# Optimization experiments

Measured on AMD Instinct MI355X. Metric: run time of the kernel, lower is better.

## Reference

```python
import jax, jax.numpy as jnp
import numpy as np

H = 12          # num heads
D = 768         # hidden size
DH = D // H     # size per head
FF = 3072       # intermediate size
EPS = 1e-11


def gelu(x):
    # tanh approximation, matching the TF source exactly
    c = np.sqrt(2.0 / np.pi).astype(np.float32)
    return x * 0.5 * (1.0 + jnp.tanh(c * (x + 0.044715 * jnp.power(x, 3))))


def layer_norm(x, gamma, beta):
    mean = jnp.mean(x, axis=-1, keepdims=True)
    var = jnp.mean(jnp.square(x - mean), axis=-1, keepdims=True)
    return (x - mean) * jax.lax.rsqrt(var + EPS) * gamma + beta


def setup_inputs() -> dict:
    key = jax.random.key(0)
    ks = jax.random.split(key, 12)
    B, S = 16, 512
    std = 0.02
    inp = {
        "x": jax.random.normal(ks[0], (B, S, D), jnp.float32),
        "mask": jnp.ones((B, S), dtype=bool),
        "Wq": jax.random.normal(ks[1], (D, D), jnp.float32) * std,
        "bq": jnp.zeros((D,), jnp.float32),
        "Wk": jax.random.normal(ks[2], (D, D), jnp.float32) * std,
        "bk": jnp.zeros((D,), jnp.float32),
        "Wv": jax.random.normal(ks[3], (D, D), jnp.float32) * std,
        "bv": jnp.zeros((D,), jnp.float32),
        "Wo": jax.random.normal(ks[4], (D, D), jnp.float32) * std,
        "bo": jnp.zeros((D,), jnp.float32),
        "g1": jnp.ones((D,), jnp.float32),
        "b1": jnp.zeros((D,), jnp.float32),
        "Wi": jax.random.normal(ks[5], (D, FF), jnp.float32) * std,
        "bi": jnp.zeros((FF,), jnp.float32),
        "Wo2": jax.random.normal(ks[6], (FF, D), jnp.float32) * std,
        "bo2": jnp.zeros((D,), jnp.float32),
        "g2": jnp.ones((D,), jnp.float32),
        "b2": jnp.zeros((D,), jnp.float32),
    }
    return inp


def reference(x, mask, Wq, bq, Wk, bk, Wv, bv, Wo, bo, g1, b1, Wi, bi, Wo2, bo2, g2, b2):
    B, S, _ = x.shape
    # QKV projections
    q = (x @ Wq + bq).reshape(B, S, H, DH)
    k = (x @ Wk + bk).reshape(B, S, H, DH)
    v = (x @ Wv + bv).reshape(B, S, H, DH)
    # scaled dot-product attention scores [B, H, S, S]
    scores = jnp.einsum("bqhd,bkhd->bhqk", q, k) / np.sqrt(DH).astype(np.float32)
    # key-side mask, applied as score * m + (1 - m) * -100 (per original source)
    m = mask[:, None, None, :].astype(jnp.float32)
    scores = scores * m + (1.0 - m) * (-100.0)
    probs = jax.nn.softmax(scores, axis=-1)
    attn = jnp.einsum("bhqk,bkhd->bqhd", probs, v).reshape(B, S, D)
    # tf.boolean_mask with all-True mask -> flatten batch and seq dims
    attn = attn.reshape(B * S, D)
    x_flat = x.reshape(B * S, D)
    # attention output projection + residual + LN
    attn_out = layer_norm(attn @ Wo + bo + x_flat, g1, b1)
    # FFN: gelu dense then output dense + residual + LN
    inter = gelu(attn_out @ Wi + bi)
    out = layer_norm(inter @ Wo2 + bo2 + attn_out, g2, b2)
    return out
```

## Files before the change

### kernel.cpp

```cpp
#include <hip/hip_runtime.h>


#define DEV __device__ __forceinline__

typedef unsigned short u16;
typedef unsigned int   u32;
typedef __bf16 bf16x8 __attribute__((ext_vector_type(8)));
typedef float  f32x4  __attribute__((ext_vector_type(4)));
typedef unsigned short u16x8 __attribute__((ext_vector_type(8)));
typedef unsigned short u16x4 __attribute__((ext_vector_type(4)));

DEV u16 f2bf(float f) {
    u32 u = __builtin_bit_cast(u32, f);
    u += 0x7fffu + ((u >> 16) & 1u);
    return (u16)(u >> 16);
}

DEV float gelu_f(float x) {
    float u = 0.7978845608028654f * (x + 0.044715f * x * x * x);
    float e = __expf(2.f * u);
    return 0.5f * x * (2.f - 2.f / (e + 1.f));
}

DEV void gload16(const void* gsrc, void* ldst) {
    __builtin_amdgcn_global_load_lds(
        (__attribute__((address_space(1))) void*)(void*)(const_cast<void*>(gsrc)),
        (__attribute__((address_space(3))) void*)ldst, 16, 0, 0);
}

DEV f32x4 MFMA(bf16x8 a, bf16x8 b, f32x4 c) {
    return __builtin_amdgcn_mfma_f32_16x16x32_bf16(a, b, c, 0, 0, 0);
}

__global__ __launch_bounds__(256) void cvt_bf16(const float* __restrict__ in,
                                                u16* __restrict__ out, int n) {
    int i = (blockIdx.x * 256 + threadIdx.x) * 4;
    if (i >= n) return;
    f32x4 v = *(const f32x4*)(in + i);
    u16x4 o;
    o.x = f2bf(v.x); o.y = f2bf(v.y); o.z = f2bf(v.z); o.w = f2bf(v.w);
    *(u16x4*)(out + i) = o;
}

__global__ __launch_bounds__(256) void transpose_cvt(const float* __restrict__ in,
                                                     u16* __restrict__ out,
                                                     int R, int C) {
    __shared__ float tile[32][33];
    int tx = threadIdx.x & 31, ty = threadIdx.x >> 5;
    int r0 = blockIdx.y * 32, c0 = blockIdx.x * 32;
#pragma unroll
    for (int i = 0; i < 4; i++)
        tile[ty + i * 8][tx] = in[(size_t)(r0 + ty + i * 8) * C + c0 + tx];
    __syncthreads();
#pragma unroll
    for (int i = 0; i < 4; i++)
        out[(size_t)(c0 + ty + i * 8) * R + r0 + tx] = f2bf(tile[tx][ty + i * 8]);
}

__global__ void concat_bias(const float* __restrict__ bq, const float* __restrict__ bk,
                            const float* __restrict__ bv, float* __restrict__ o) {
    int i = blockIdx.x * 256 + threadIdx.x;
    if (i < 2304) o[i] = (i < 768) ? bq[i] : (i < 1536 ? bk[i - 768] : bv[i - 1536]);
}

template <int EPI>
__global__ __launch_bounds__(256) void gemm_bt(const u16* __restrict__ A,
                                               const u16* __restrict__ BT,
                                               const float* __restrict__ bias,
                                               void* __restrict__ Cout,
                                               int N, int K) {
    __shared__ __align__(16) char smem[32768];
    const int t = threadIdx.x, lane = t & 63, wid = t >> 6;
    const int tm = blockIdx.y, tn = blockIdx.x;
    const int wm = wid >> 1, wn = wid & 1;

    f32x4 acc[4][4];
#pragma unroll
    for (int i = 0; i < 4; i++)
#pragma unroll
        for (int j = 0; j < 4; j++) acc[i][j] = f32x4{0.f, 0.f, 0.f, 0.f};

    const u16* Ab = A + (size_t)tm * 128 * K;
    const u16* Bb = BT + (size_t)tn * 128 * K;
    char* As = smem;
    char* Bs = smem + 16384;

    for (int kt = 0; kt < K; kt += 64) {
        __syncthreads();
#pragma unroll
        for (int i = 0; i < 4; i++) {
            int cw = wid * 4 + i;
            int o = cw * 1024 + lane * 16;
            int row = o >> 7;
            int cb = (o & 127) ^ ((row & 7) << 4);
            gload16(Ab + (size_t)row * K + kt + (cb >> 1), As + cw * 1024);
            gload16(Bb + (size_t)row * K + kt + (cb >> 1), Bs + cw * 1024);
        }
        __syncthreads();
#pragma unroll
        for (int ks = 0; ks < 2; ++ks) {
            bf16x8 af[4], bfr[4];
#pragma unroll
            for (int mi = 0; mi < 4; mi++) {
                int row = wm * 64 + mi * 16 + (lane & 15);
                int cb = (ks * 64 + ((lane >> 4) << 4)) ^ ((row & 7) << 4);
                af[mi] = *(const bf16x8*)(As + row * 128 + cb);
            }
#pragma unroll
            for (int ni = 0; ni < 4; ni++) {
                int row = wn * 64 + ni * 16 + (lane & 15);
                int cb = (ks * 64 + ((lane >> 4) << 4)) ^ ((row & 7) << 4);
                bfr[ni] = *(const bf16x8*)(Bs + row * 128 + cb);
            }
#pragma unroll
            for (int mi = 0; mi < 4; mi++)
#pragma unroll
                for (int ni = 0; ni < 4; ni++)
                    acc[mi][ni] = MFMA(af[mi], bfr[ni], acc[mi][ni]);
        }
    }

    const int r0 = tm * 128 + wm * 64, c0 = tn * 128 + wn * 64;
    float bcol[4];
#pragma unroll
    for (int ni = 0; ni < 4; ni++) bcol[ni] = bias[c0 + ni * 16 + (lane & 15)];
#pragma unroll
    for (int mi = 0; mi < 4; mi++) {
#pragma unroll
        for (int r = 0; r < 4; r++) {
            int gr = r0 + mi * 16 + ((lane >> 4) << 2) + r;
#pragma unroll
            for (int ni = 0; ni < 4; ni++) {
                int gc = c0 + ni * 16 + (lane & 15);
                float v = acc[mi][ni][r] + bcol[ni];
                if constexpr (EPI == 2) v = gelu_f(v);
                if constexpr (EPI == 1)
                    ((float*)Cout)[(size_t)gr * N + gc] = v;
                else
                    ((u16*)Cout)[(size_t)gr * N + gc] = f2bf(v);
            }
        }
    }
}

__global__ __launch_bounds__(256) void attn_kernel(const u16* __restrict__ QKV,
                                                   u16* __restrict__ attnb) {
    __shared__ __align__(16) char sm[24576];
    char* Ks = sm;
    char* Vt = sm + 8192;
    const int t = threadIdx.x, lane = t & 63, wid = t >> 6;
    const int qt = blockIdx.x, bh = blockIdx.y;
    const int b = bh / 12, h = bh % 12;
    const size_t base = (size_t)b * 512 * 2304;
    char* Pw = sm + 16384 + wid * 2048;

    bf16x8 aq[2];
    {
        int qrow = qt * 64 + wid * 16 + (lane & 15);
        const u16* qp = QKV + base + (size_t)qrow * 2304 + h * 64 + ((lane >> 4) << 3);
        aq[0] = *(const bf16x8*)qp;
        aq[1] = *(const bf16x8*)(qp + 32);
    }
    f32x4 oacc[4];
#pragma unroll
    for (int g = 0; g < 4; g++) oacc[g] = f32x4{0.f, 0.f, 0.f, 0.f};
    float mrun[4] = {-1e30f, -1e30f, -1e30f, -1e30f};
    float lrun[4] = {0.f, 0.f, 0.f, 0.f};

    for (int kt = 0; kt < 8; ++kt) {
        __syncthreads();
#pragma unroll
        for (int i = 0; i < 2; i++) {
            int cw = wid * 2 + i;
            int o = cw * 1024 + lane * 16;
            int row = o >> 7;
            int cb = (o & 127) ^ ((row & 7) << 4);
            gload16(QKV + base + (size_t)(kt * 64 + row) * 2304 + 768 + h * 64 + (cb >> 1),
                    Ks + cw * 1024);
        }
        {
            int key = t & 63, dh0 = wid * 16;
            const u16* vp = QKV + base + (size_t)(kt * 64 + key) * 2304 + 1536 + h * 64 + dh0;
            u16x8 v0 = *(const u16x8*)vp;
            u16x8 v1 = *(const u16x8*)(vp + 8);
#pragma unroll
            for (int j = 0; j < 8; j++) {
                int dh = dh0 + j;
                *(u16*)(Vt + dh * 128 + ((key * 2) ^ ((dh & 7) << 4))) = v0[j];
            }
#pragma unroll
            for (int j = 0; j < 8; j++) {
                int dh = dh0 + 8 + j;
                *(u16*)(Vt + dh * 128 + ((key * 2) ^ ((dh & 7) << 4))) = v1[j];
            }
        }
        __syncthreads();

        f32x4 sacc[4];
#pragma unroll
        for (int ni = 0; ni < 4; ni++) sacc[ni] = f32x4{0.f, 0.f, 0.f, 0.f};
#pragma unroll
        for (int ni = 0; ni < 4; ni++) {
            int row = ni * 16 + (lane & 15);
#pragma unroll
            for (int ks = 0; ks < 2; ks++) {
                int cb = (ks * 64 + ((lane >> 4) << 4)) ^ ((row & 7) << 4);
                bf16x8 bk = *(const bf16x8*)(Ks + row * 128 + cb);
                sacc[ni] = MFMA(aq[ks], bk, sacc[ni]);
            }
        }
#pragma unroll
        for (int ni = 0; ni < 4; ni++)
#pragma unroll
            for (int r = 0; r < 4; r++) sacc[ni][r] *= 0.125f;

#pragma unroll
        for (int r = 0; r < 4; r++) {
            float pm = fmaxf(fmaxf(sacc[0][r], sacc[1][r]), fmaxf(sacc[2][r], sacc[3][r]));
            pm = fmaxf(pm, __shfl_xor(pm, 1));
            pm = fmaxf(pm, __shfl_xor(pm, 2));
            pm = fmaxf(pm, __shfl_xor(pm, 4));
            pm = fmaxf(pm, __shfl_xor(pm, 8));
            float mnew = fmaxf(mrun[r], pm);
            float sf = __expf(mrun[r] - mnew);
            mrun[r] = mnew;
            lrun[r] *= sf;
#pragma unroll
            for (int g = 0; g < 4; g++) oacc[g][r] *= sf;
            int prow = ((lane >> 4) << 2) + r;
            float ps = 0.f;
#pragma unroll
            for (int ni = 0; ni < 4; ni++) {
                float p = __expf(sacc[ni][r] - mnew);
                ps += p;
                int col = ni * 16 + (lane & 15);
                *(u16*)(Pw + prow * 128 + ((col * 2) ^ ((prow & 7) << 4))) = f2bf(p);
            }
            ps += __shfl_xor(ps, 1);
            ps += __shfl_xor(ps, 2);
            ps += __shfl_xor(ps, 4);
            ps += __shfl_xor(ps, 8);
            lrun[r] += ps;
        }
        __syncthreads();

#pragma unroll
        for (int ks = 0; ks < 2; ks++) {
            int prow = lane & 15;
            int pcb = (ks * 64 + ((lane >> 4) << 4)) ^ ((prow & 7) << 4);
            bf16x8 ap = *(const bf16x8*)(Pw + prow * 128 + pcb);
#pragma unroll
            for (int g = 0; g < 4; g++) {
                int vrow = g * 16 + (lane & 15);
                int vcb = (ks * 64 + ((lane >> 4) << 4)) ^ ((vrow & 7) << 4);
                bf16x8 bv = *(const bf16x8*)(Vt + vrow * 128 + vcb);
                oacc[g] = MFMA(ap, bv, oacc[g]);
            }
        }
    }

#pragma unroll
    for (int g = 0; g < 4; g++)
#pragma unroll
        for (int r = 0; r < 4; r++) {
            int qrow = qt * 64 + wid * 16 + ((lane >> 4) << 2) + r;
            float o = oacc[g][r] / lrun[r];
            attnb[(size_t)(b * 512 + qrow) * 768 + h * 64 + g * 16 + (lane & 15)] = f2bf(o);
        }
}

__global__ __launch_bounds__(256) void ln_kernel(const float* __restrict__ Y,
                                                 const float* __restrict__ res,
                                                 const float* __restrict__ g,
                                                 const float* __restrict__ bta,
                                                 float* __restrict__ outf,
                                                 u16* __restrict__ outb) {
    int row = blockIdx.x, t = threadIdx.x, lane = t & 63, wid = t >> 6;
    const float* y = Y + (size_t)row * 768;
    const float* rr = res + (size_t)row * 768;
    float v[3];
#pragma unroll
    for (int i = 0; i < 3; i++) v[i] = y[t + i * 256] + rr[t + i * 256];

    float s = v[0] + v[1] + v[2];
#pragma unroll
    for (int o = 32; o; o >>= 1) s += __shfl_xor(s, o);
    __shared__ float sm[4];
    __shared__ float bc[2];
    if (lane == 0) sm[wid] = s;
    __syncthreads();
    if (t == 0) bc[0] = (sm[0] + sm[1] + sm[2] + sm[3]) * (1.f / 768.f);
    __syncthreads();
    float mean = bc[0];

    float q = 0.f;
#pragma unroll
    for (int i = 0; i < 3; i++) { float d = v[i] - mean; q += d * d; }
#pragma unroll
    for (int o = 32; o; o >>= 1) q += __shfl_xor(q, o);
    if (lane == 0) sm[wid] = q;
    __syncthreads();
    if (t == 0) bc[1] = rsqrtf((sm[0] + sm[1] + sm[2] + sm[3]) * (1.f / 768.f) + 1e-11f);
    __syncthreads();
    float rs = bc[1];
#pragma unroll
    for (int i = 0; i < 3; i++) {
        int c = t + i * 256;
        float o = (v[i] - mean) * rs * g[c] + bta[c];
        outf[(size_t)row * 768 + c] = o;
        if (outb) outb[(size_t)row * 768 + c] = f2bf(o);
    }
}

extern "C" void kernel_launch(void* const* d_in, const int* in_sizes, int n_in,
                              void* d_out, int out_size, void* d_ws, size_t ws_size,
                              hipStream_t stream) {
    const float* x   = (const float*)d_in[0];
    const float* Wq  = (const float*)d_in[2];
    const float* bq  = (const float*)d_in[3];
    const float* Wk  = (const float*)d_in[4];
    const float* bk  = (const float*)d_in[5];
    const float* Wv  = (const float*)d_in[6];
    const float* bv  = (const float*)d_in[7];
    const float* Wo  = (const float*)d_in[8];
    const float* bo  = (const float*)d_in[9];
    const float* g1  = (const float*)d_in[10];
    const float* b1  = (const float*)d_in[11];
    const float* Wi  = (const float*)d_in[12];
    const float* bi  = (const float*)d_in[13];
    const float* Wo2 = (const float*)d_in[14];
    const float* bo2 = (const float*)d_in[15];
    const float* g2  = (const float*)d_in[16];
    const float* b2  = (const float*)d_in[17];

    char* w = (char*)d_ws;
    size_t off = 0;
    auto alloc = [&](size_t n) { size_t o = off; off += (n + 255) & ~(size_t)255; return o; };
    size_t oXb    = alloc((size_t)8192 * 768 * 2);
    size_t oWqkvT = alloc((size_t)2304 * 768 * 2);
    size_t oWoT   = alloc((size_t)768 * 768 * 2);
    size_t oWiT   = alloc((size_t)3072 * 768 * 2);
    size_t oWo2T  = alloc((size_t)768 * 3072 * 2);
    size_t oBqkv  = alloc((size_t)2304 * 4);
    size_t oR0    = alloc((size_t)8192 * 3072 * 2);
    size_t oY     = alloc((size_t)8192 * 768 * 4);
    size_t oAof   = alloc((size_t)8192 * 768 * 4);
    size_t oAob   = alloc((size_t)8192 * 768 * 2);
    (void)ws_size; (void)in_sizes; (void)n_in; (void)out_size;

    u16*   Xb    = (u16*)(w + oXb);
    u16*   WqkvT = (u16*)(w + oWqkvT);
    u16*   WoT   = (u16*)(w + oWoT);
    u16*   WiT   = (u16*)(w + oWiT);
    u16*   Wo2T  = (u16*)(w + oWo2T);
    float* bqkv  = (float*)(w + oBqkv);
    u16*   QKV   = (u16*)(w + oR0);
    u16*   attnb = (u16*)(w + oR0 + (size_t)8192 * 2304 * 2);
    u16*   inter = (u16*)(w + oR0);
    float* Y     = (float*)(w + oY);
    float* aof   = (float*)(w + oAof);
    u16*   aob   = (u16*)(w + oAob);

    cvt_bf16<<<6144, 256, 0, stream>>>(x, Xb, 8192 * 768);
    transpose_cvt<<<dim3(24, 24), 256, 0, stream>>>(Wq, WqkvT, 768, 768);
    transpose_cvt<<<dim3(24, 24), 256, 0, stream>>>(Wk, WqkvT + 768 * 768, 768, 768);
    transpose_cvt<<<dim3(24, 24), 256, 0, stream>>>(Wv, WqkvT + 2 * 768 * 768, 768, 768);
    transpose_cvt<<<dim3(24, 24), 256, 0, stream>>>(Wo, WoT, 768, 768);
    transpose_cvt<<<dim3(96, 24), 256, 0, stream>>>(Wi, WiT, 768, 3072);
    transpose_cvt<<<dim3(24, 96), 256, 0, stream>>>(Wo2, Wo2T, 3072, 768);
    concat_bias<<<9, 256, 0, stream>>>(bq, bk, bv, bqkv);

    gemm_bt<0><<<dim3(18, 64), 256, 0, stream>>>(Xb, WqkvT, bqkv, QKV, 2304, 768);
    attn_kernel<<<dim3(8, 192), 256, 0, stream>>>(QKV, attnb);
    gemm_bt<1><<<dim3(6, 64), 256, 0, stream>>>(attnb, WoT, bo, Y, 768, 768);
    ln_kernel<<<8192, 256, 0, stream>>>(Y, x, g1, b1, aof, aob);
    gemm_bt<2><<<dim3(24, 64), 256, 0, stream>>>(aob, WiT, bi, inter, 3072, 768);
    gemm_bt<1><<<dim3(6, 64), 256, 0, stream>>>(inter, Wo2T, bo2, Y, 768, 3072);
    ln_kernel<<<8192, 256, 0, stream>>>(Y, aof, g2, b2, (float*)d_out, nullptr);
}
```

Baseline: 310.3 us.

## Double-buffer GEMM LDS tiles, swizzle workgroup order, raise MFMA priority

The GEMM kernel now keeps two LDS stages, so the next K-tile's global-to-LDS load is issued while MFMAs run on the current one, and each iteration has one barrier instead of two. The grid is flattened to 1D with an XCD-aware remap of block IDs to tiles, aiming for better L2 reuse across the chiplets. s_setprio is raised around the MFMA loop. LDS use doubles to 64KB per block, which may reduce how many blocks fit on a CU.

Result: faster. 281.1 us (-9.4%).

```diff
diff --git a/kernel.cpp b/kernel.cpp
--- a/kernel.cpp
+++ b/kernel.cpp
@@ -68,10 +68,12 @@
                                                const u16* __restrict__ BT,
                                                const float* __restrict__ bias,
                                                void* __restrict__ Cout,
-                                               int N, int K) {
-    __shared__ __align__(16) char smem[32768];
+                                               int N, int K, int ntn) {
+    __shared__ __align__(16) char smem[65536];
     const int t = threadIdx.x, lane = t & 63, wid = t >> 6;
-    const int tm = blockIdx.y, tn = blockIdx.x;
+    const int nwg = gridDim.x, bid = blockIdx.x;
+    const int swz = ((nwg & 7) == 0) ? ((bid & 7) * (nwg >> 3) + (bid >> 3)) : bid;
+    const int tm = swz / ntn, tn = swz % ntn;
     const int wm = wid >> 1, wn = wid & 1;
 
     f32x4 acc[4][4];
@@ -82,21 +84,31 @@
 
     const u16* Ab = A + (size_t)tm * 128 * K;
     const u16* Bb = BT + (size_t)tn * 128 * K;
-    char* As = smem;
-    char* Bs = smem + 16384;
-
-    for (int kt = 0; kt < K; kt += 64) {
-        __syncthreads();
-#pragma unroll
-        for (int i = 0; i < 4; i++) {
-            int cw = wid * 4 + i;
-            int o = cw * 1024 + lane * 16;
-            int row = o >> 7;
-            int cb = (o & 127) ^ ((row & 7) << 4);
-            gload16(Ab + (size_t)row * K + kt + (cb >> 1), As + cw * 1024);
-            gload16(Bb + (size_t)row * K + kt + (cb >> 1), Bs + cw * 1024);
-        }
-        __syncthreads();
+    const int so = lane * 16;
+    const int srin = so >> 7;
+    const int scol = ((so & 127) ^ ((srin & 7) << 4)) >> 1;
+
+#define STG(KT, BUF)                                                          \
+    {                                                                         \
+        char* As_ = smem + (BUF) * 32768;                                     \
+        char* Bs_ = As_ + 16384;                                              \
+        _Pragma("unroll")                                                     \
+        for (int i_ = 0; i_ < 4; i_++) {                                      \
+            int cw_ = wid * 4 + i_;                                           \
+            int row_ = cw_ * 8 + srin;                                        \
+            gload16(Ab + (size_t)row_ * K + (KT) + scol, As_ + cw_ * 1024);   \
+            gload16(Bb + (size_t)row_ * K + (KT) + scol, Bs_ + cw_ * 1024);   \
+        }                                                                     \
+    }
+
+    const int NT = K >> 6;
+    STG(0, 0);
+    __syncthreads();
+
+    for (int k = 0; k < NT; ++k) {
+        if (k + 1 < NT) STG((k + 1) << 6, (k & 1) ^ 1);
+        const char* As = smem + (k & 1) * 32768;
+        const char* Bs = As + 16384;
 #pragma unroll
         for (int ks = 0; ks < 2; ++ks) {
             bf16x8 af[4], bfr[4];
@@ -112,13 +124,17 @@
                 int cb = (ks * 64 + ((lane >> 4) << 4)) ^ ((row & 7) << 4);
                 bfr[ni] = *(const bf16x8*)(Bs + row * 128 + cb);
             }
+            __builtin_amdgcn_s_setprio(1);
 #pragma unroll
             for (int mi = 0; mi < 4; mi++)
 #pragma unroll
                 for (int ni = 0; ni < 4; ni++)
                     acc[mi][ni] = MFMA(af[mi], bfr[ni], acc[mi][ni]);
-        }
-    }
+            __builtin_amdgcn_s_setprio(0);
+        }
+        __syncthreads();
+    }
+#undef STG
 
     const int r0 = tm * 128 + wm * 64, c0 = tn * 128 + wn * 64;
     float bcol[4];
@@ -370,11 +386,11 @@
     transpose_cvt<<<dim3(24, 96), 256, 0, stream>>>(Wo2, Wo2T, 3072, 768);
     concat_bias<<<9, 256, 0, stream>>>(bq, bk, bv, bqkv);
 
-    gemm_bt<0><<<dim3(18, 64), 256, 0, stream>>>(Xb, WqkvT, bqkv, QKV, 2304, 768);
+    gemm_bt<0><<<1152, 256, 0, stream>>>(Xb, WqkvT, bqkv, QKV, 2304, 768, 18);
     attn_kernel<<<dim3(8, 192), 256, 0, stream>>>(QKV, attnb);
-    gemm_bt<1><<<dim3(6, 64), 256, 0, stream>>>(attnb, WoT, bo, Y, 768, 768);
+    gemm_bt<1><<<384, 256, 0, stream>>>(attnb, WoT, bo, Y, 768, 768, 6);
     ln_kernel<<<8192, 256, 0, stream>>>(Y, x, g1, b1, aof, aob);
-    gemm_bt<2><<<dim3(24, 64), 256, 0, stream>>>(aob, WiT, bi, inter, 3072, 768);
-    gemm_bt<1><<<dim3(6, 64), 256, 0, stream>>>(inter, Wo2T, bo2, Y, 768, 3072);
+    gemm_bt<2><<<1536, 256, 0, stream>>>(aob, WiT, bi, inter, 3072, 768, 24);
+    gemm_bt<1><<<384, 256, 0, stream>>>(inter, Wo2T, bo2, Y, 768, 3072, 6);
     ln_kernel<<<8192, 256, 0, stream>>>(Y, aof, g2, b2, (float*)d_out, nullptr);
 }
```

## Replace 128x128 GEMM with 256x256-tile multi-stage pipelined GEMM and XCD swizzle

Applied to the files above, without the earlier changes.

Replaces the 128x128-tile, 256-thread GEMM with a 256x256-tile, 512-thread kernel. It uses a 4-deep LDS ring of K=32 slices filled by async global-to-LDS loads, with explicit vmcnt waits and raw barriers so loads overlap the MFMA work. The kernel also remaps block IDs across XCDs for L2 locality and raises wave priority around MFMA bursts. The aim is more data reuse per tile and hidden load latency. The trade-off is that the N=768 GEMMs now launch only 96 blocks, which leaves many CUs idle and may cancel the gains there.

New measurement: 333.5 us. +7.5%, slower.

```diff
diff --git a/kernel.cpp b/kernel.cpp
--- a/kernel.cpp
+++ b/kernel.cpp
@@ -64,75 +64,118 @@
 }
 
 template <int EPI>
-__global__ __launch_bounds__(256) void gemm_bt(const u16* __restrict__ A,
-                                               const u16* __restrict__ BT,
-                                               const float* __restrict__ bias,
-                                               void* __restrict__ Cout,
-                                               int N, int K) {
-    __shared__ __align__(16) char smem[32768];
+__global__ __launch_bounds__(512, 2) void gemm256(const u16* __restrict__ A,
+                                                  const u16* __restrict__ BT,
+                                                  const float* __restrict__ bias,
+                                                  void* __restrict__ Cout,
+                                                  int N, int K, int ntn) {
+    __shared__ __align__(16) char smem[131072];
     const int t = threadIdx.x, lane = t & 63, wid = t >> 6;
-    const int tm = blockIdx.y, tn = blockIdx.x;
-    const int wm = wid >> 1, wn = wid & 1;
-
-    f32x4 acc[4][4];
-#pragma unroll
-    for (int i = 0; i < 4; i++)
-#pragma unroll
-        for (int j = 0; j < 4; j++) acc[i][j] = f32x4{0.f, 0.f, 0.f, 0.f};
-
-    const u16* Ab = A + (size_t)tm * 128 * K;
-    const u16* Bb = BT + (size_t)tn * 128 * K;
-    char* As = smem;
-    char* Bs = smem + 16384;
-
-    for (int kt = 0; kt < K; kt += 64) {
-        __syncthreads();
-#pragma unroll
-        for (int i = 0; i < 4; i++) {
-            int cw = wid * 4 + i;
-            int o = cw * 1024 + lane * 16;
-            int row = o >> 7;
-            int cb = (o & 127) ^ ((row & 7) << 4);
-            gload16(Ab + (size_t)row * K + kt + (cb >> 1), As + cw * 1024);
-            gload16(Bb + (size_t)row * K + kt + (cb >> 1), Bs + cw * 1024);
-        }
-        __syncthreads();
-#pragma unroll
-        for (int ks = 0; ks < 2; ++ks) {
-            bf16x8 af[4], bfr[4];
-#pragma unroll
-            for (int mi = 0; mi < 4; mi++) {
-                int row = wm * 64 + mi * 16 + (lane & 15);
-                int cb = (ks * 64 + ((lane >> 4) << 4)) ^ ((row & 7) << 4);
-                af[mi] = *(const bf16x8*)(As + row * 128 + cb);
-            }
-#pragma unroll
-            for (int ni = 0; ni < 4; ni++) {
-                int row = wn * 64 + ni * 16 + (lane & 15);
-                int cb = (ks * 64 + ((lane >> 4) << 4)) ^ ((row & 7) << 4);
-                bfr[ni] = *(const bf16x8*)(Bs + row * 128 + cb);
-            }
-#pragma unroll
-            for (int mi = 0; mi < 4; mi++)
-#pragma unroll
-                for (int ni = 0; ni < 4; ni++)
-                    acc[mi][ni] = MFMA(af[mi], bfr[ni], acc[mi][ni]);
-        }
-    }
-
-    const int r0 = tm * 128 + wm * 64, c0 = tn * 128 + wn * 64;
-    float bcol[4];
-#pragma unroll
-    for (int ni = 0; ni < 4; ni++) bcol[ni] = bias[c0 + ni * 16 + (lane & 15)];
-#pragma unroll
-    for (int mi = 0; mi < 4; mi++) {
+    const int nwg = gridDim.x, bid = blockIdx.x;
+    const int swzb = ((nwg & 7) == 0) ? ((bid & 7) * (nwg >> 3) + (bid >> 3)) : bid;
+    const int tm = swzb / ntn, tn = swzb % ntn;
+    const int wm = wid >> 2, wn = wid & 3;
+
+    f32x4 acc[8][4];
+#pragma unroll
+    for (int m = 0; m < 8; m++)
+#pragma unroll
+        for (int n = 0; n < 4; n++) acc[m][n] = f32x4{0.f, 0.f, 0.f, 0.f};
+
+    const int HN = K >> 5;
+    const u16* Ab = A + (size_t)tm * 256 * K;
+    const u16* Bb = BT + (size_t)tn * 256 * K;
+
+    int rj[2], kbj[2];
+#pragma unroll
+    for (int j = 0; j < 2; j++) {
+        int X = j * 8192 + wid * 1024 + lane * 16;
+        int Y = X ^ (((X >> 7) & 7) << 4);
+        rj[j] = Y >> 6;
+        kbj[j] = (Y & 63) >> 1;
+    }
+    const u16* pA0 = Ab + (size_t)rj[0] * K + kbj[0];
+    const u16* pA1 = Ab + (size_t)rj[1] * K + kbj[1];
+    const u16* pB0 = Bb + (size_t)rj[0] * K + kbj[0];
+    const u16* pB1 = Bb + (size_t)rj[1] * K + kbj[1];
+
+    const int g16 = (lane >> 4) << 4;
+    const int rA = wm * 128 + (lane & 15);
+    const int rB = wn * 64 + (lane & 15);
+    const int baseA = (rA * 64 + g16) ^ (((rA >> 1) & 7) << 4);
+    const int baseB = (rB * 64 + g16) ^ (((rB >> 1) & 7) << 4);
+
+#define STGA(X)                                                        \
+    {                                                                  \
+        char* d_ = smem + ((X) & 3) * 32768 + wid * 1024;              \
+        gload16(pA0 + (X) * 32, d_);                                   \
+        gload16(pA1 + (X) * 32, d_ + 8192);                            \
+    }
+#define STGB(X)                                                        \
+    {                                                                  \
+        char* d_ = smem + ((X) & 3) * 32768 + 16384 + wid * 1024;      \
+        gload16(pB0 + (X) * 32, d_);                                   \
+        gload16(pB1 + (X) * 32, d_ + 8192);                            \
+    }
+
+    STGA(0) STGB(0) STGA(1) STGB(1) STGA(2) STGB(2)
+    asm volatile("s_waitcnt vmcnt(8)" ::: "memory");
+    __builtin_amdgcn_s_barrier();
+    asm volatile("" ::: "memory");
+
+    for (int h = 0; h < HN; ++h) {
+        const char* sa = smem + (h & 3) * 32768;
+        const char* sb = sa + 16384;
+        bf16x8 af[4], bfr[4];
+#pragma unroll
+        for (int mi = 0; mi < 4; mi++) af[mi] = *(const bf16x8*)(sa + baseA + mi * 1024);
+#pragma unroll
+        for (int ni = 0; ni < 4; ni++) bfr[ni] = *(const bf16x8*)(sb + baseB + ni * 1024);
+        if (h + 3 < HN) STGA(h + 3)
+        __builtin_amdgcn_s_setprio(1);
+#pragma unroll
+        for (int mi = 0; mi < 4; mi++)
+#pragma unroll
+            for (int ni = 0; ni < 4; ni++)
+                acc[mi][ni] = MFMA(af[mi], bfr[ni], acc[mi][ni]);
+        __builtin_amdgcn_s_setprio(0);
+        __builtin_amdgcn_s_barrier();
+        asm volatile("" ::: "memory");
+#pragma unroll
+        for (int mi = 0; mi < 4; mi++) af[mi] = *(const bf16x8*)(sa + baseA + 4096 + mi * 1024);
+        if (h + 3 < HN) STGB(h + 3)
+        __builtin_amdgcn_s_setprio(1);
+#pragma unroll
+        for (int mi = 0; mi < 4; mi++)
+#pragma unroll
+            for (int ni = 0; ni < 4; ni++)
+                acc[4 + mi][ni] = MFMA(af[mi], bfr[ni], acc[4 + mi][ni]);
+        __builtin_amdgcn_s_setprio(0);
+        if (h + 1 < HN) {
+            int ahead = HN - 2 - h;
+            if (ahead >= 2)      asm volatile("s_waitcnt vmcnt(8)" ::: "memory");
+            else if (ahead == 1) asm volatile("s_waitcnt vmcnt(4)" ::: "memory");
+            else                 asm volatile("s_waitcnt vmcnt(0)" ::: "memory");
+        }
+        __builtin_amdgcn_s_barrier();
+        asm volatile("" ::: "memory");
+    }
+#undef STGA
+#undef STGB
+
+    const int r0 = tm * 256 + wm * 128, c0 = tn * 256 + wn * 64;
+    float cb[4];
+#pragma unroll
+    for (int ni = 0; ni < 4; ni++) cb[ni] = bias[c0 + ni * 16 + (lane & 15)];
+#pragma unroll
+    for (int m = 0; m < 8; m++) {
 #pragma unroll
         for (int r = 0; r < 4; r++) {
-            int gr = r0 + mi * 16 + ((lane >> 4) << 2) + r;
+            int gr = r0 + m * 16 + ((lane >> 4) << 2) + r;
 #pragma unroll
             for (int ni = 0; ni < 4; ni++) {
                 int gc = c0 + ni * 16 + (lane & 15);
-                float v = acc[mi][ni][r] + bcol[ni];
+                float v = acc[m][ni][r] + cb[ni];
                 if constexpr (EPI == 2) v = gelu_f(v);
                 if constexpr (EPI == 1)
                     ((float*)Cout)[(size_t)gr * N + gc] = v;
@@ -370,11 +413,11 @@
     transpose_cvt<<<dim3(24, 96), 256, 0, stream>>>(Wo2, Wo2T, 3072, 768);
     concat_bias<<<9, 256, 0, stream>>>(bq, bk, bv, bqkv);
 
-    gemm_bt<0><<<dim3(18, 64), 256, 0, stream>>>(Xb, WqkvT, bqkv, QKV, 2304, 768);
+    gemm256<0><<<288, 512, 0, stream>>>(Xb, WqkvT, bqkv, QKV, 2304, 768, 9);
     attn_kernel<<<dim3(8, 192), 256, 0, stream>>>(QKV, attnb);
-    gemm_bt<1><<<dim3(6, 64), 256, 0, stream>>>(attnb, WoT, bo, Y, 768, 768);
+    gemm256<1><<<96, 512, 0, stream>>>(attnb, WoT, bo, Y, 768, 768, 3);
     ln_kernel<<<8192, 256, 0, stream>>>(Y, x, g1, b1, aof, aob);
-    gemm_bt<2><<<dim3(24, 64), 256, 0, stream>>>(aob, WiT, bi, inter, 3072, 768);
-    gemm_bt<1><<<dim3(6, 64), 256, 0, stream>>>(inter, Wo2T, bo2, Y, 768, 3072);
+    gemm256<2><<<384, 512, 0, stream>>>(aob, WiT, bi, inter, 3072, 768, 12);
+    gemm256<1><<<96, 512, 0, stream>>>(inter, Wo2T, bo2, Y, 768, 3072, 3);
     ln_kernel<<<8192, 256, 0, stream>>>(Y, aof, g2, b2, (float*)d_out, nullptr);
 }
```

## Replace GEMM with 128x256-tile triple-buffered pipelined kernel and XCD block swizzle

Applied to the files above, without the earlier changes.

Replaces the 128x128, 256-thread, single-buffered GEMM with a 512-thread kernel that computes 128x256 tiles. Global-to-LDS loads for the next two K-steps are issued ahead into a three-stage LDS ring, using vmcnt waits and raw barriers, while raising wave priority around the MFMA block. Tile indices come from a 1D grid remapped so neighbouring blocks land on the same XCD, which is meant to improve L2 reuse. The larger tiles need about 144KB of LDS, which limits occupancy to one block per CU. The N=768 GEMMs also drop to 192 blocks, fewer than the number of CUs.

Measured after the change: 299.3 us. -3.5%, faster.

```diff
diff --git a/kernel.cpp b/kernel.cpp
--- a/kernel.cpp
+++ b/kernel.cpp
@@ -64,15 +64,17 @@
 }
 
 template <int EPI>
-__global__ __launch_bounds__(256) void gemm_bt(const u16* __restrict__ A,
-                                               const u16* __restrict__ BT,
-                                               const float* __restrict__ bias,
-                                               void* __restrict__ Cout,
-                                               int N, int K) {
-    __shared__ __align__(16) char smem[32768];
+__global__ __launch_bounds__(512, 2) void gemm_p3(const u16* __restrict__ A,
+                                                  const u16* __restrict__ BT,
+                                                  const float* __restrict__ bias,
+                                                  void* __restrict__ Cout,
+                                                  int N, int K, int ntn) {
+    __shared__ __align__(16) char smem[147456];
     const int t = threadIdx.x, lane = t & 63, wid = t >> 6;
-    const int tm = blockIdx.y, tn = blockIdx.x;
-    const int wm = wid >> 1, wn = wid & 1;
+    const int nwg = gridDim.x, bid = blockIdx.x;
+    const int swzb = ((nwg & 7) == 0) ? ((bid & 7) * (nwg >> 3) + (bid >> 3)) : bid;
+    const int tm = swzb / ntn, tn = swzb % ntn;
+    const int wm = wid >> 2, wn = wid & 3;
 
     f32x4 acc[4][4];
 #pragma unroll
@@ -80,50 +82,91 @@
 #pragma unroll
         for (int j = 0; j < 4; j++) acc[i][j] = f32x4{0.f, 0.f, 0.f, 0.f};
 
+    const int NT = K >> 6;
     const u16* Ab = A + (size_t)tm * 128 * K;
-    const u16* Bb = BT + (size_t)tn * 128 * K;
-    char* As = smem;
-    char* Bs = smem + 16384;
-
-    for (int kt = 0; kt < K; kt += 64) {
-        __syncthreads();
-#pragma unroll
-        for (int i = 0; i < 4; i++) {
-            int cw = wid * 4 + i;
-            int o = cw * 1024 + lane * 16;
-            int row = o >> 7;
-            int cb = (o & 127) ^ ((row & 7) << 4);
-            gload16(Ab + (size_t)row * K + kt + (cb >> 1), As + cw * 1024);
-            gload16(Bb + (size_t)row * K + kt + (cb >> 1), Bs + cw * 1024);
-        }
-        __syncthreads();
-#pragma unroll
-        for (int ks = 0; ks < 2; ++ks) {
-            bf16x8 af[4], bfr[4];
-#pragma unroll
-            for (int mi = 0; mi < 4; mi++) {
-                int row = wm * 64 + mi * 16 + (lane & 15);
-                int cb = (ks * 64 + ((lane >> 4) << 4)) ^ ((row & 7) << 4);
-                af[mi] = *(const bf16x8*)(As + row * 128 + cb);
-            }
-#pragma unroll
-            for (int ni = 0; ni < 4; ni++) {
-                int row = wn * 64 + ni * 16 + (lane & 15);
-                int cb = (ks * 64 + ((lane >> 4) << 4)) ^ ((row & 7) << 4);
-                bfr[ni] = *(const bf16x8*)(Bs + row * 128 + cb);
-            }
-#pragma unroll
-            for (int mi = 0; mi < 4; mi++)
-#pragma unroll
-                for (int ni = 0; ni < 4; ni++)
-                    acc[mi][ni] = MFMA(af[mi], bfr[ni], acc[mi][ni]);
-        }
-    }
-
-    const int r0 = tm * 128 + wm * 64, c0 = tn * 128 + wn * 64;
-    float bcol[4];
-#pragma unroll
-    for (int ni = 0; ni < 4; ni++) bcol[ni] = bias[c0 + ni * 16 + (lane & 15)];
+    const u16* Bb = BT + (size_t)tn * 256 * K;
+
+    const int dst0 = wid * 1024, dst1 = dst0 + 8192;
+    int srow[2], scol[2];
+#pragma unroll
+    for (int j = 0; j < 2; j++) {
+        int X = wid * 1024 + lane * 16 + j * 8192;
+        int row = X >> 7;
+        int cb = (X & 127) ^ ((row & 7) << 4);
+        srow[j] = row; scol[j] = cb >> 1;
+    }
+    const u16* pA0  = Ab + (size_t)srow[0] * K + scol[0];
+    const u16* pA1  = Ab + (size_t)srow[1] * K + scol[1];
+    const u16* pB00 = Bb + (size_t)srow[0] * K + scol[0];
+    const u16* pB01 = Bb + (size_t)srow[1] * K + scol[1];
+    const u16* pB10 = Bb + (size_t)(128 + srow[0]) * K + scol[0];
+    const u16* pB11 = Bb + (size_t)(128 + srow[1]) * K + scol[1];
+
+    const int swz = (lane & 7) << 4, g16 = (lane >> 4) << 4;
+    int aoff[2], boff[2];
+#pragma unroll
+    for (int p = 0; p < 2; p++) {
+        int cx = (p * 64 + g16) ^ swz;
+        aoff[p] = wm * 8192 + (lane & 15) * 128 + cx;
+        boff[p] = 16384 + (wn >> 1) * 16384 + (wn & 1) * 8192 + (lane & 15) * 128 + cx;
+    }
+
+#define STG(TT)                                                               \
+    {                                                                         \
+        char* bb_ = smem + ((TT) % 3) * 49152;                                \
+        int ko_ = (TT) * 64;                                                  \
+        gload16(pA0 + ko_, bb_ + dst0);                                       \
+        gload16(pA1 + ko_, bb_ + dst1);                                       \
+        gload16(pB00 + ko_, bb_ + 16384 + dst0);                              \
+        gload16(pB01 + ko_, bb_ + 16384 + dst1);                              \
+        gload16(pB10 + ko_, bb_ + 32768 + dst0);                              \
+        gload16(pB11 + ko_, bb_ + 32768 + dst1);                              \
+    }
+
+    STG(0) STG(1)
+    asm volatile("s_waitcnt vmcnt(6)" ::: "memory");
+    __builtin_amdgcn_s_barrier();
+    asm volatile("" ::: "memory");
+
+    for (int tt = 0; tt < NT; ++tt) {
+        const char* buf = smem + (tt % 3) * 49152;
+        if (tt + 2 < NT) STG(tt + 2)
+        bf16x8 a0[4], b0[4], a1[4], b1[4];
+#pragma unroll
+        for (int mi = 0; mi < 4; mi++) a0[mi] = *(const bf16x8*)(buf + aoff[0] + mi * 2048);
+#pragma unroll
+        for (int ni = 0; ni < 4; ni++) b0[ni] = *(const bf16x8*)(buf + boff[0] + ni * 2048);
+#pragma unroll
+        for (int mi = 0; mi < 4; mi++) a1[mi] = *(const bf16x8*)(buf + aoff[1] + mi * 2048);
+#pragma unroll
+        for (int ni = 0; ni < 4; ni++) b1[ni] = *(const bf16x8*)(buf + boff[1] + ni * 2048);
+        __builtin_amdgcn_s_barrier();
+        asm volatile("" ::: "memory");
+        __builtin_amdgcn_s_setprio(1);
+#pragma unroll
+        for (int mi = 0; mi < 4; mi++)
+#pragma unroll
+            for (int ni = 0; ni < 4; ni++)
+                acc[mi][ni] = MFMA(a0[mi], b0[ni], acc[mi][ni]);
+#pragma unroll
+        for (int mi = 0; mi < 4; mi++)
+#pragma unroll
+            for (int ni = 0; ni < 4; ni++)
+                acc[mi][ni] = MFMA(a1[mi], b1[ni], acc[mi][ni]);
+        __builtin_amdgcn_s_setprio(0);
+        if (tt + 1 < NT) {
+            if (tt + 2 < NT) asm volatile("s_waitcnt vmcnt(6)" ::: "memory");
+            else             asm volatile("s_waitcnt vmcnt(0)" ::: "memory");
+        }
+        __builtin_amdgcn_s_barrier();
+        asm volatile("" ::: "memory");
+    }
+#undef STG
+
+    const int r0 = tm * 128 + wm * 64, c0 = tn * 256 + wn * 64;
+    float cb[4];
+#pragma unroll
+    for (int ni = 0; ni < 4; ni++) cb[ni] = bias[c0 + ni * 16 + (lane & 15)];
 #pragma unroll
     for (int mi = 0; mi < 4; mi++) {
 #pragma unroll
@@ -132,7 +175,7 @@
 #pragma unroll
             for (int ni = 0; ni < 4; ni++) {
                 int gc = c0 + ni * 16 + (lane & 15);
-                float v = acc[mi][ni][r] + bcol[ni];
+                float v = acc[mi][ni][r] + cb[ni];
                 if constexpr (EPI == 2) v = gelu_f(v);
                 if constexpr (EPI == 1)
                     ((float*)Cout)[(size_t)gr * N + gc] = v;
@@ -370,11 +413,11 @@
     transpose_cvt<<<dim3(24, 96), 256, 0, stream>>>(Wo2, Wo2T, 3072, 768);
     concat_bias<<<9, 256, 0, stream>>>(bq, bk, bv, bqkv);
 
-    gemm_bt<0><<<dim3(18, 64), 256, 0, stream>>>(Xb, WqkvT, bqkv, QKV, 2304, 768);
+    gemm_p3<0><<<576, 512, 0, stream>>>(Xb, WqkvT, bqkv, QKV, 2304, 768, 9);
     attn_kernel<<<dim3(8, 192), 256, 0, stream>>>(QKV, attnb);
-    gemm_bt<1><<<dim3(6, 64), 256, 0, stream>>>(attnb, WoT, bo, Y, 768, 768);
+    gemm_p3<1><<<192, 512, 0, stream>>>(attnb, WoT, bo, Y, 768, 768, 3);
     ln_kernel<<<8192, 256, 0, stream>>>(Y, x, g1, b1, aof, aob);
-    gemm_bt<2><<<dim3(24, 64), 256, 0, stream>>>(aob, WiT, bi, inter, 3072, 768);
-    gemm_bt<1><<<dim3(6, 64), 256, 0, stream>>>(inter, Wo2T, bo2, Y, 768, 3072);
+    gemm_p3<2><<<768, 512, 0, stream>>>(aob, WiT, bi, inter, 3072, 768, 12);
+    gemm_p3<1><<<192, 512, 0, stream>>>(inter, Wo2T, bo2, Y, 768, 3072, 3);
     ln_kernel<<<8192, 256, 0, stream>>>(Y, aof, g2, b2, (float*)d_out, nullptr);
 }
```
